# Kernel tuning notes

Measured on AMD Instinct MI355X. Metric: run time of the kernel, lower is better.

The kernel has to match this reference:

```python
import jax, jax.numpy as jnp
import numpy as np

N_NODES = 50000
N_EDGES = 640000  # directed; edges (2i, 2i+1) are mutual reverses
NODE_DIM = 128
EDGE_DIM = 16
UNITS = 128
EDGE_STEPS = 4
NODE_STEPS = 4


def setup_inputs() -> dict:
    key = jax.random.key(0)
    ks = jax.random.split(key, 8)
    n_pairs = N_EDGES // 2
    a = jax.random.randint(ks[0], (n_pairs,), 0, N_NODES, dtype=jnp.int32)
    b = jax.random.randint(ks[1], (n_pairs,), 0, N_NODES, dtype=jnp.int32)
    # interleave so edge 2i = a->b and edge 2i+1 = b->a (reverse pair)
    edge_src = jnp.stack([a, b], axis=1).reshape(-1)
    edge_dst = jnp.stack([b, a], axis=1).reshape(-1)
    rev_edge = (jnp.arange(N_EDGES, dtype=jnp.int32) ^ 1)
    node_feature = jax.random.normal(ks[2], (N_NODES, NODE_DIM), jnp.float32)
    edge_feature = jax.random.normal(ks[3], (N_EDGES, EDGE_DIM), jnp.float32)
    d_in = NODE_DIM + EDGE_DIM
    W_init = jax.random.normal(ks[4], (d_in, UNITS), jnp.float32) / np.sqrt(d_in)
    b_init = jnp.zeros((UNITS,), jnp.float32)
    W_upd = jax.random.normal(ks[5], (UNITS, UNITS), jnp.float32) / np.sqrt(UNITS)
    b_upd = jnp.zeros((UNITS,), jnp.float32)
    d_node_out = UNITS + NODE_DIM
    W_node = jax.random.normal(ks[6], (d_node_out, d_node_out), jnp.float32) / np.sqrt(d_node_out)
    b_node = jnp.zeros((d_node_out,), jnp.float32)
    epsilon = jnp.zeros((), jnp.float32)
    return dict(node_feature=node_feature, edge_feature=edge_feature,
                edge_src=edge_src, edge_dst=edge_dst, rev_edge=rev_edge,
                W_init=W_init, b_init=b_init, W_upd=W_upd, b_upd=b_upd,
                W_node=W_node, b_node=b_node, epsilon=epsilon)


def reference(node_feature, edge_feature, edge_src, edge_dst, rev_edge,
              W_init, b_init, W_upd, b_upd, W_node, b_node, epsilon):
    N = node_feature.shape[0]
    # initial edge projection: concat(src node feat, edge feat) -> units, relu
    h = jax.nn.relu(
        jnp.concatenate([node_feature[edge_src], edge_feature], axis=-1) @ W_init + b_init
    )  # [E, units]
    # directed edge message passing (D-MPNN style)
    for _ in range(EDGE_STEPS):
        agg = jax.ops.segment_sum(h, edge_dst, num_segments=N)        # [N, units]
        message = agg[edge_src] - h[rev_edge]                          # exclude reverse edge
        h = jax.nn.relu(message @ W_upd + b_upd + h)
    # aggregate edges to nodes, concat with original node features
    msg = jax.ops.segment_sum(h, edge_dst, num_segments=N)             # [N, units]
    x = jnp.concatenate([node_feature, msg], axis=-1)                  # [N, units+node_dim]
    x0 = (x * (1.0 + epsilon)) @ W_node + b_node                       # GIN-style initial
    # node message passing: sum-aggregate neighbors + residual initial
    for _ in range(NODE_STEPS):
        x = jax.ops.segment_sum(x[edge_src], edge_dst, num_segments=N) + x0
    return x
```

## Files before the change

### kernel.cpp

```cpp
#include <hip/hip_runtime.h>
#include <stdint.h>

#define N_NODES 50000
#define N_EDGES 640000
#define NODE_DIM 128
#define EDGE_DIM 16
#define UNITS 128
#define DOUT 256
#define SCAN_NB ((N_NODES + 255) / 256)

typedef __attribute__((ext_vector_type(4))) float v4f;
typedef __attribute__((ext_vector_type(8))) short v8s;
typedef __attribute__((ext_vector_type(4))) short v4s;
typedef __attribute__((ext_vector_type(2))) unsigned v2u;
typedef __attribute__((ext_vector_type(4))) unsigned v4u;

static __device__ __forceinline__ short f2bf(float f) {
    return (short)((__float_as_uint(f) + 0x8000u) >> 16);
}
static __device__ __forceinline__ float bf2f(short s) {
    return __uint_as_float(((unsigned)(unsigned short)s) << 16);
}
static __device__ __forceinline__ unsigned pack_bf2(float a, float b) {
    unsigned ua = __float_as_uint(a) + 0x8000u;
    unsigned ub = __float_as_uint(b) + 0x8000u;
    return __builtin_amdgcn_perm(ub, ua, 0x07060302);
}

__global__ void k_zero(int* __restrict__ p, int n) {
    int i = blockIdx.x * 256 + threadIdx.x;
    if (i < n) p[i] = 0;
}

__global__ void k_hist(const int* __restrict__ dst, int* __restrict__ counts) {
    int e = blockIdx.x * 256 + threadIdx.x;
    if (e < N_EDGES) atomicAdd(&counts[dst[e]], 1);
}

__global__ __launch_bounds__(256) void k_scan_part(const int* __restrict__ counts,
                                                   int* __restrict__ part) {
    __shared__ int red[256];
    int t = threadIdx.x;
    int i = blockIdx.x * 256 + t;
    red[t] = (i < N_NODES) ? counts[i] : 0;
    __syncthreads();
#pragma unroll
    for (int s = 128; s > 0; s >>= 1) {
        if (t < s) red[t] += red[t + s];
        __syncthreads();
    }
    if (t == 0) part[blockIdx.x] = red[0];
}

__global__ __launch_bounds__(256) void k_scan_base(const int* __restrict__ part,
                                                   int* __restrict__ base) {
    __shared__ int buf[2][256];
    int t = threadIdx.x;
    int v = (t < SCAN_NB) ? part[t] : 0;
    buf[0][t] = v;
    __syncthreads();
    int cur = 0;
#pragma unroll
    for (int s = 1; s < 256; s <<= 1) {
        int nv = buf[cur][t];
        if (t >= s) nv += buf[cur][t - s];
        buf[cur ^ 1][t] = nv;
        cur ^= 1;
        __syncthreads();
    }
    if (t < SCAN_NB) base[t] = buf[cur][t] - v;
}

__global__ __launch_bounds__(256) void k_scan_write(const int* __restrict__ counts,
                                                    const int* __restrict__ base,
                                                    int* __restrict__ rowptr,
                                                    int* __restrict__ cursor) {
    __shared__ int buf[2][256];
    int t = threadIdx.x;
    int i = blockIdx.x * 256 + t;
    int v = (i < N_NODES) ? counts[i] : 0;
    buf[0][t] = v;
    __syncthreads();
    int cur = 0;
#pragma unroll
    for (int s = 1; s < 256; s <<= 1) {
        int nv = buf[cur][t];
        if (t >= s) nv += buf[cur][t - s];
        buf[cur ^ 1][t] = nv;
        cur ^= 1;
        __syncthreads();
    }
    if (i < N_NODES) {
        int excl = buf[cur][t] - v + base[blockIdx.x];
        rowptr[i] = excl;
        cursor[i] = excl;
    }
    if (i == 0) rowptr[N_NODES] = N_EDGES;
}

__global__ void k_fill(const int* __restrict__ src, const int* __restrict__ dst,
                       int* __restrict__ cursor, int* __restrict__ csr_eid,
                       int* __restrict__ csr_src) {
    int e = blockIdx.x * 256 + threadIdx.x;
    if (e < N_EDGES) {
        int d = dst[e];
        int pos = atomicAdd(&cursor[d], 1);
        csr_eid[pos] = e;
        csr_src[pos] = src[e];
    }
}

__global__ void k_prep(const float* __restrict__ Wi, const float* __restrict__ Wu,
                       const float* __restrict__ Wn, short* __restrict__ WtI1,
                       short* __restrict__ WtI2, short* __restrict__ WtU,
                       short* __restrict__ WtN) {
    int i = blockIdx.x * 256 + threadIdx.x;
    if (i < 128 * 128) {
        int n = i >> 7, k = i & 127;
        WtI1[i] = f2bf(Wi[k * UNITS + n]);
        return;
    }
    int j = i - 128 * 128;
    if (j < 128 * 32) {
        int n = j >> 5, k = j & 31;
        WtI2[j] = (k < EDGE_DIM) ? f2bf(Wi[(NODE_DIM + k) * UNITS + n]) : (short)0;
        return;
    }
    int l = j - 128 * 32;
    if (l < 128 * 128) {
        int n = l >> 7, k = l & 127;
        WtU[l] = f2bf(Wu[k * UNITS + n]);
        return;
    }
    int m = l - 128 * 128;
    if (m < 256 * 256) {
        int n = m >> 8, k = m & 255;
        WtN[m] = f2bf(Wn[k * DOUT + n]);
    }
}

__global__ __launch_bounds__(256) void k_nfw(
    const float* __restrict__ nf, const short* __restrict__ WtI1,
    short* __restrict__ nfw) {
    __shared__ __align__(16) short nT[32][UNITS + 8];
    int t = threadIdx.x;
    int i0 = blockIdx.x * 32;
#pragma unroll
    for (int i = 0; i < 4; ++i) {
        int idx = i * 256 + t;
        int row = idx >> 5, c4 = idx & 31;
        int ri = i0 + row; if (ri >= N_NODES) ri = N_NODES - 1;
        v4f v = *(const v4f*)&nf[(size_t)ri * NODE_DIM + c4 * 4];
        unsigned* dst = (unsigned*)&nT[row][c4 * 4];
        dst[0] = pack_bf2(v[0], v[1]);
        dst[1] = pack_bf2(v[2], v[3]);
    }
    __syncthreads();
    int w = t >> 6, lane = t & 63, quad = lane >> 4, l16 = lane & 15;
    v4f acc[2][2];
#pragma unroll
    for (int m = 0; m < 2; ++m)
#pragma unroll
        for (int n = 0; n < 2; ++n) { acc[m][n][0] = 0; acc[m][n][1] = 0; acc[m][n][2] = 0; acc[m][n][3] = 0; }
#pragma unroll
    for (int kc = 0; kc < 4; ++kc) {
        int ko = kc * 32 + quad * 8;
        v8s a0 = *(const v8s*)&nT[l16][ko];
        v8s a1 = *(const v8s*)&nT[16 + l16][ko];
        v8s b0 = *(const v8s*)&WtI1[(size_t)(w * 32 + l16) * UNITS + ko];
        v8s b1 = *(const v8s*)&WtI1[(size_t)(w * 32 + 16 + l16) * UNITS + ko];
        acc[0][0] = __builtin_amdgcn_mfma_f32_16x16x32_bf16(a0, b0, acc[0][0], 0, 0, 0);
        acc[1][0] = __builtin_amdgcn_mfma_f32_16x16x32_bf16(a1, b0, acc[1][0], 0, 0, 0);
        acc[0][1] = __builtin_amdgcn_mfma_f32_16x16x32_bf16(a0, b1, acc[0][1], 0, 0, 0);
        acc[1][1] = __builtin_amdgcn_mfma_f32_16x16x32_bf16(a1, b1, acc[1][1], 0, 0, 0);
    }
#pragma unroll
    for (int m = 0; m < 2; ++m)
#pragma unroll
        for (int n = 0; n < 2; ++n)
#pragma unroll
            for (int r = 0; r < 4; ++r) {
                int row = m * 16 + quad * 4 + r;
                int col = w * 32 + n * 16 + l16;
                if (i0 + row < N_NODES)
                    nfw[(size_t)(i0 + row) * UNITS + col] = f2bf(acc[m][n][r]);
            }
}

__global__ __launch_bounds__(256) void k_edge_init2(
    const float* __restrict__ ef, const int* __restrict__ esrc,
    const short* __restrict__ nfw, const short* __restrict__ WtI2,
    const float* __restrict__ bi, short* __restrict__ h) {
    __shared__ __align__(16) short efT[32][40];
    __shared__ __align__(16) short nfwT[32][UNITS + 8];
    __shared__ int srcT[32];
    int t = threadIdx.x;
    int e0 = blockIdx.x * 32;
    if (t < 32) srcT[t] = esrc[e0 + t];
    if (t < 128) {
        int row = t >> 2, c4 = t & 3;
        v4f v = *(const v4f*)&ef[(size_t)(e0 + row) * EDGE_DIM + c4 * 4];
        unsigned* dst = (unsigned*)&efT[row][c4 * 4];
        dst[0] = pack_bf2(v[0], v[1]);
        dst[1] = pack_bf2(v[2], v[3]);
        unsigned* z = (unsigned*)&efT[row][16 + c4 * 4];
        z[0] = 0; z[1] = 0;
    }
    __syncthreads();
#pragma unroll
    for (int i = 0; i < 2; ++i) {
        int idx = i * 256 + t;
        int row = idx >> 4, c = idx & 15;
        v8s v = *(const v8s*)&nfw[(size_t)srcT[row] * UNITS + c * 8];
        *((v8s*)&nfwT[row][c * 8]) = v;
    }
    __syncthreads();
    int w = t >> 6, lane = t & 63, quad = lane >> 4, l16 = lane & 15;
    v4f acc[2][2];
#pragma unroll
    for (int m = 0; m < 2; ++m)
#pragma unroll
        for (int n = 0; n < 2; ++n) { acc[m][n][0] = 0; acc[m][n][1] = 0; acc[m][n][2] = 0; acc[m][n][3] = 0; }
    {
        int ko = quad * 8;
        v8s a0 = *(const v8s*)&efT[l16][ko];
        v8s a1 = *(const v8s*)&efT[16 + l16][ko];
        v8s b0 = *(const v8s*)&WtI2[(size_t)(w * 32 + l16) * 32 + ko];
        v8s b1 = *(const v8s*)&WtI2[(size_t)(w * 32 + 16 + l16) * 32 + ko];
        acc[0][0] = __builtin_amdgcn_mfma_f32_16x16x32_bf16(a0, b0, acc[0][0], 0, 0, 0);
        acc[1][0] = __builtin_amdgcn_mfma_f32_16x16x32_bf16(a1, b0, acc[1][0], 0, 0, 0);
        acc[0][1] = __builtin_amdgcn_mfma_f32_16x16x32_bf16(a0, b1, acc[0][1], 0, 0, 0);
        acc[1][1] = __builtin_amdgcn_mfma_f32_16x16x32_bf16(a1, b1, acc[1][1], 0, 0, 0);
    }
#pragma unroll
    for (int m = 0; m < 2; ++m)
#pragma unroll
        for (int n = 0; n < 2; ++n)
#pragma unroll
            for (int r = 0; r < 4; ++r) {
                int row = m * 16 + quad * 4 + r;
                int col = w * 32 + n * 16 + l16;
                float v = acc[m][n][r] + bf2f(nfwT[row][col]) + bi[col];
                h[(size_t)(e0 + row) * UNITS + col] = f2bf(fmaxf(v, 0.f));
            }
}

__global__ __launch_bounds__(256) void k_agg_bf(
    const short* __restrict__ h, const int* __restrict__ rowptr,
    const int* __restrict__ csr_eid, short* __restrict__ aggb) {
    int w = threadIdx.x >> 6, lane = threadIdx.x & 63;
    int node = blockIdx.x * 4 + w;
    int g = lane >> 4, l = lane & 15;
    int beg = rowptr[node], end = rowptr[node + 1];
    float a[8];
#pragma unroll
    for (int k = 0; k < 8; ++k) a[k] = 0.f;
    for (int j = beg + g; j < end; j += 4) {
        int eid = csr_eid[j];
        v8s u = *(const v8s*)&h[(size_t)eid * UNITS + l * 8];
#pragma unroll
        for (int k = 0; k < 8; ++k) a[k] += bf2f(u[k]);
    }
#pragma unroll
    for (int k = 0; k < 8; ++k) {
        a[k] += __shfl_xor(a[k], 16);
        a[k] += __shfl_xor(a[k], 32);
    }
    if (g == 0) {
        v4u o;
        o[0] = pack_bf2(a[0], a[1]); o[1] = pack_bf2(a[2], a[3]);
        o[2] = pack_bf2(a[4], a[5]); o[3] = pack_bf2(a[6], a[7]);
        *((v4u*)&aggb[(size_t)node * UNITS + l * 8]) = o;
    }
}

__global__ __launch_bounds__(256) void k_agg(
    const short* __restrict__ h, const int* __restrict__ rowptr,
    const int* __restrict__ csr_eid, float* __restrict__ agg) {
    int w = threadIdx.x >> 6, lane = threadIdx.x & 63;
    int node = blockIdx.x * 4 + w;
    int g = lane >> 4, l = lane & 15;
    int beg = rowptr[node], end = rowptr[node + 1];
    float a[8];
#pragma unroll
    for (int k = 0; k < 8; ++k) a[k] = 0.f;
    for (int j = beg + g; j < end; j += 4) {
        int eid = csr_eid[j];
        v8s u = *(const v8s*)&h[(size_t)eid * UNITS + l * 8];
#pragma unroll
        for (int k = 0; k < 8; ++k) a[k] += bf2f(u[k]);
    }
#pragma unroll
    for (int k = 0; k < 8; ++k) {
        a[k] += __shfl_xor(a[k], 16);
        a[k] += __shfl_xor(a[k], 32);
    }
    if (g == 0) {
        v4f o0, o1;
        o0[0] = a[0]; o0[1] = a[1]; o0[2] = a[2]; o0[3] = a[3];
        o1[0] = a[4]; o1[1] = a[5]; o1[2] = a[6]; o1[3] = a[7];
        *((v4f*)&agg[(size_t)node * UNITS + l * 8]) = o0;
        *((v4f*)&agg[(size_t)node * UNITS + l * 8 + 4]) = o1;
    }
}

__global__ __launch_bounds__(256, 4) void k_edge_step(
    const short* __restrict__ aggb, const int* __restrict__ esrc,
    const short* __restrict__ WtU, const float* __restrict__ bu,
    short* __restrict__ h) {
    __shared__ __align__(16) short hT[64][UNITS + 8];
    __shared__ __align__(16) short msgT[64][UNITS + 8];
    int t = threadIdx.x;
    int e0 = blockIdx.x * 64;
    int srcv[4];
#pragma unroll
    for (int i = 0; i < 4; ++i) srcv[i] = esrc[e0 + ((i * 256 + t) >> 4)];
    v8s hreg[4], areg[4];
#pragma unroll
    for (int i = 0; i < 4; ++i) {
        int idx = i * 256 + t;
        int row = idx >> 4, c = idx & 15;
        hreg[i] = *(const v8s*)&h[(size_t)(e0 + row) * UNITS + c * 8];
        areg[i] = *(const v8s*)&aggb[(size_t)srcv[i] * UNITS + c * 8];
    }
#pragma unroll
    for (int i = 0; i < 4; ++i) {
        int idx = i * 256 + t;
        int row = idx >> 4, c = idx & 15;
        *((v8s*)&hT[row][c * 8]) = hreg[i];
    }
    __syncthreads();
#pragma unroll
    for (int i = 0; i < 4; ++i) {
        int idx = i * 256 + t;
        int row = idx >> 4, c = idx & 15;
        v8s hr = *(const v8s*)&hT[row ^ 1][c * 8];
        unsigned* mrow = (unsigned*)&msgT[row][c * 8];
#pragma unroll
        for (int k = 0; k < 4; ++k) {
            float d0 = bf2f(areg[i][2 * k]) - bf2f(hr[2 * k]);
            float d1 = bf2f(areg[i][2 * k + 1]) - bf2f(hr[2 * k + 1]);
            mrow[k] = pack_bf2(d0, d1);
        }
    }
    __syncthreads();
    int w = t >> 6, lane = t & 63, quad = lane >> 4, l16 = lane & 15;
    v4f acc[4][2];
#pragma unroll
    for (int m = 0; m < 4; ++m)
#pragma unroll
        for (int n = 0; n < 2; ++n) { acc[m][n][0] = 0; acc[m][n][1] = 0; acc[m][n][2] = 0; acc[m][n][3] = 0; }
#pragma unroll
    for (int kc = 0; kc < 4; ++kc) {
        int ko = kc * 32 + quad * 8;
        v8s b0 = *(const v8s*)&WtU[(size_t)(w * 32 + l16) * UNITS + ko];
        v8s b1 = *(const v8s*)&WtU[(size_t)(w * 32 + 16 + l16) * UNITS + ko];
#pragma unroll
        for (int m = 0; m < 4; ++m) {
            v8s a = *(const v8s*)&msgT[m * 16 + l16][ko];
            acc[m][0] = __builtin_amdgcn_mfma_f32_16x16x32_bf16(a, b0, acc[m][0], 0, 0, 0);
            acc[m][1] = __builtin_amdgcn_mfma_f32_16x16x32_bf16(a, b1, acc[m][1], 0, 0, 0);
        }
    }
#pragma unroll
    for (int m = 0; m < 4; ++m)
#pragma unroll
        for (int n = 0; n < 2; ++n)
#pragma unroll
            for (int r = 0; r < 4; ++r) {
                int row = m * 16 + quad * 4 + r;
                int col = w * 32 + n * 16 + l16;
                float v = acc[m][n][r] + bu[col] + bf2f(hT[row][col]);
                hT[row][col] = f2bf(fmaxf(v, 0.f));
            }
    __syncthreads();
#pragma unroll
    for (int i = 0; i < 4; ++i) {
        int idx = i * 256 + t;
        int row = idx >> 4, c = idx & 15;
        *((v8s*)&h[(size_t)(e0 + row) * UNITS + c * 8]) = *(const v8s*)&hT[row][c * 8];
    }
}

__global__ __launch_bounds__(256) void k_node_init(
    const float* __restrict__ nf, const float* __restrict__ msg,
    const short* __restrict__ WtN, const float* __restrict__ bn,
    const float* __restrict__ epsv, float* __restrict__ x0,
    short* __restrict__ xcatb) {
    __shared__ __align__(16) short xin[32][DOUT + 8];
    int t = threadIdx.x;
    int i0 = blockIdx.x * 32;
#pragma unroll
    for (int i = 0; i < 8; ++i) {
        int idx = i * 256 + t;
        int row = idx >> 6, c4 = idx & 63;
        int ri = i0 + row; if (ri >= N_NODES) ri = N_NODES - 1;
        int col = c4 * 4;
        v4f v;
        if (col < NODE_DIM) v = *(const v4f*)&nf[(size_t)ri * NODE_DIM + col];
        else v = *(const v4f*)&msg[(size_t)ri * UNITS + (col - NODE_DIM)];
        unsigned* dst = (unsigned*)&xin[row][col];
        dst[0] = pack_bf2(v[0], v[1]);
        dst[1] = pack_bf2(v[2], v[3]);
    }
    __syncthreads();
#pragma unroll
    for (int i = 0; i < 4; ++i) {
        int idx = i * 256 + t;
        int row = idx >> 5, c = idx & 31;
        int ri = i0 + row;
        if (ri < N_NODES) {
            v8s v = *(const v8s*)&xin[row][c * 8];
            *((v8s*)&xcatb[(size_t)ri * DOUT + c * 8]) = v;
        }
    }
    int w = t >> 6, lane = t & 63, quad = lane >> 4, l16 = lane & 15;
    v4f acc[2][4];
#pragma unroll
    for (int m = 0; m < 2; ++m)
#pragma unroll
        for (int n = 0; n < 4; ++n) { acc[m][n][0] = 0; acc[m][n][1] = 0; acc[m][n][2] = 0; acc[m][n][3] = 0; }
#pragma unroll
    for (int kc = 0; kc < 8; ++kc) {
        int ko = kc * 32 + quad * 8;
        v8s a0 = *(const v8s*)&xin[l16][ko];
        v8s a1 = *(const v8s*)&xin[16 + l16][ko];
#pragma unroll
        for (int n = 0; n < 4; ++n) {
            v8s b = *(const v8s*)&WtN[(size_t)(w * 64 + n * 16 + l16) * DOUT + ko];
            acc[0][n] = __builtin_amdgcn_mfma_f32_16x16x32_bf16(a0, b, acc[0][n], 0, 0, 0);
            acc[1][n] = __builtin_amdgcn_mfma_f32_16x16x32_bf16(a1, b, acc[1][n], 0, 0, 0);
        }
    }
    float scale = 1.f + epsv[0];
#pragma unroll
    for (int m = 0; m < 2; ++m)
#pragma unroll
        for (int n = 0; n < 4; ++n)
#pragma unroll
            for (int r = 0; r < 4; ++r) {
                int row = m * 16 + quad * 4 + r;
                int col = w * 64 + n * 16 + l16;
                if (i0 + row < N_NODES)
                    x0[(size_t)(i0 + row) * DOUT + col] = acc[m][n][r] * scale + bn[col];
            }
}

__global__ __launch_bounds__(256) void k_node_step_b(
    const short* __restrict__ xb, const float* __restrict__ x0,
    const int* __restrict__ rowptr, const int* __restrict__ csr_src,
    short* __restrict__ outb, float* __restrict__ outf, int writef) {
    int w = threadIdx.x >> 6, lane = threadIdx.x & 63;
    int node = blockIdx.x * 4 + w;
    int beg = rowptr[node], end = rowptr[node + 1];
    v4f xv = *(const v4f*)&x0[(size_t)node * DOUT + lane * 4];
    float a0 = xv[0], a1 = xv[1], a2 = xv[2], a3 = xv[3];
    float b0 = 0, b1 = 0, b2 = 0, b3 = 0;
    int j = beg;
    for (; j + 2 <= end; j += 2) {
        int s0 = csr_src[j], s1 = csr_src[j + 1];
        v4s u = *(const v4s*)&xb[(size_t)s0 * DOUT + lane * 4];
        v4s v = *(const v4s*)&xb[(size_t)s1 * DOUT + lane * 4];
        a0 += bf2f(u[0]); a1 += bf2f(u[1]); a2 += bf2f(u[2]); a3 += bf2f(u[3]);
        b0 += bf2f(v[0]); b1 += bf2f(v[1]); b2 += bf2f(v[2]); b3 += bf2f(v[3]);
    }
    if (j < end) {
        v4s u = *(const v4s*)&xb[(size_t)csr_src[j] * DOUT + lane * 4];
        a0 += bf2f(u[0]); a1 += bf2f(u[1]); a2 += bf2f(u[2]); a3 += bf2f(u[3]);
    }
    a0 += b0; a1 += b1; a2 += b2; a3 += b3;
    if (writef) {
        v4f o; o[0] = a0; o[1] = a1; o[2] = a2; o[3] = a3;
        *((v4f*)&outf[(size_t)node * DOUT + lane * 4]) = o;
    } else {
        v2u o; o[0] = pack_bf2(a0, a1); o[1] = pack_bf2(a2, a3);
        *((v2u*)&outb[(size_t)node * DOUT + lane * 4]) = o;
    }
}

extern "C" void kernel_launch(void* const* d_in, const int* in_sizes, int n_in,
                              void* d_out, int out_size, void* d_ws, size_t ws_size,
                              hipStream_t stream) {
    const float* nf  = (const float*)d_in[0];
    const float* ef  = (const float*)d_in[1];
    const int* esrc  = (const int*)d_in[2];
    const int* edst  = (const int*)d_in[3];
    const float* Wi  = (const float*)d_in[5];
    const float* bi  = (const float*)d_in[6];
    const float* Wu  = (const float*)d_in[7];
    const float* bu  = (const float*)d_in[8];
    const float* Wn  = (const float*)d_in[9];
    const float* bn  = (const float*)d_in[10];
    const float* eps = (const float*)d_in[11];

    char* ws = (char*)d_ws;
    size_t off = 0;
    auto alloc = [&](size_t bytes) -> char* {
        char* p = ws + off;
        off += (bytes + 255) & ~(size_t)255;
        return p;
    };
    short* h     = (short*)alloc((size_t)N_EDGES * UNITS * 2);
    float* x0    = (float*)h;
    short* xcatb = (short*)((char*)h + (size_t)N_NODES * DOUT * 4);
    short* xbA   = (short*)((char*)xcatb + (size_t)N_NODES * DOUT * 2);
    short* xbB   = (short*)((char*)xbA + (size_t)N_NODES * DOUT * 2);
    char*  R     = alloc((size_t)N_NODES * UNITS * 4);
    short* nfw   = (short*)R;
    short* aggb  = (short*)(R + (size_t)N_NODES * UNITS * 2);
    float* agg   = (float*)R;
    int* counts  = (int*)alloc((size_t)N_NODES * 4);
    int* rowptr  = (int*)alloc((size_t)(N_NODES + 1) * 4);
    int* cursor  = (int*)alloc((size_t)N_NODES * 4);
    int* part    = (int*)alloc((size_t)SCAN_NB * 4);
    int* base    = (int*)alloc((size_t)SCAN_NB * 4);
    int* csr_eid = (int*)alloc((size_t)N_EDGES * 4);
    int* csr_src = (int*)alloc((size_t)N_EDGES * 4);
    short* WtI1  = (short*)alloc((size_t)128 * 128 * 2);
    short* WtI2  = (short*)alloc((size_t)128 * 32 * 2);
    short* WtU   = (short*)alloc((size_t)128 * 128 * 2);
    short* WtN   = (short*)alloc((size_t)256 * 256 * 2);
    float* xout  = (float*)d_out;

    if (ws_size < off) return;

    k_zero<<<(N_NODES + 255) / 256, 256, 0, stream>>>(counts, N_NODES);
    k_hist<<<(N_EDGES + 255) / 256, 256, 0, stream>>>(edst, counts);
    k_scan_part<<<SCAN_NB, 256, 0, stream>>>(counts, part);
    k_scan_base<<<1, 256, 0, stream>>>(part, base);
    k_scan_write<<<SCAN_NB, 256, 0, stream>>>(counts, base, rowptr, cursor);
    k_fill<<<(N_EDGES + 255) / 256, 256, 0, stream>>>(esrc, edst, cursor, csr_eid, csr_src);
    k_prep<<<(128 * 128 + 128 * 32 + 128 * 128 + 256 * 256 + 255) / 256, 256, 0, stream>>>(
        Wi, Wu, Wn, WtI1, WtI2, WtU, WtN);

    k_nfw<<<(N_NODES + 31) / 32, 256, 0, stream>>>(nf, WtI1, nfw);
    k_edge_init2<<<N_EDGES / 32, 256, 0, stream>>>(ef, esrc, nfw, WtI2, bi, h);
    for (int s = 0; s < 4; ++s) {
        k_agg_bf<<<N_NODES / 4, 256, 0, stream>>>(h, rowptr, csr_eid, aggb);
        k_edge_step<<<N_EDGES / 64, 256, 0, stream>>>(aggb, esrc, WtU, bu, h);
    }
    k_agg<<<N_NODES / 4, 256, 0, stream>>>(h, rowptr, csr_eid, agg);
    k_node_init<<<(N_NODES + 31) / 32, 256, 0, stream>>>(nf, agg, WtN, bn, eps, x0, xcatb);
    k_node_step_b<<<N_NODES / 4, 256, 0, stream>>>(xcatb, x0, rowptr, csr_src, xbA, nullptr, 0);
    k_node_step_b<<<N_NODES / 4, 256, 0, stream>>>(xbA, x0, rowptr, csr_src, xbB, nullptr, 0);
    k_node_step_b<<<N_NODES / 4, 256, 0, stream>>>(xbB, x0, rowptr, csr_src, xbA, nullptr, 0);
    k_node_step_b<<<N_NODES / 4, 256, 0, stream>>>(xbA, x0, rowptr, csr_src, nullptr, xout, 1);
}
```

Before: 1.025 ms.

## Stage GEMM outputs through LDS for coalesced stores and preload CSR indices via shuffles

k_nfw and k_edge_init2 now write their accumulator tiles to shared memory and store rows to global memory as 16-byte vectors instead of scattered 2-byte stores. k_edge_init2 also doubles its tile to 64 edges and issues its gathered neighbor loads before the edge-feature conversion. The aggregation and node-step kernels load up to 64 CSR indices in one coalesced read and broadcast them with shuffles, keeping more gathers in flight per iteration. This adds LDS traffic, extra barriers and a separate fallback path for nodes with degree above 64.

```diff
diff --git a/kernel.cpp b/kernel.cpp
--- a/kernel.cpp
+++ b/kernel.cpp
@@ -174,6 +174,7 @@
         acc[0][1] = __builtin_amdgcn_mfma_f32_16x16x32_bf16(a0, b1, acc[0][1], 0, 0, 0);
         acc[1][1] = __builtin_amdgcn_mfma_f32_16x16x32_bf16(a1, b1, acc[1][1], 0, 0, 0);
     }
+    __syncthreads();
 #pragma unroll
     for (int m = 0; m < 2; ++m)
 #pragma unroll
@@ -182,22 +183,36 @@
             for (int r = 0; r < 4; ++r) {
                 int row = m * 16 + quad * 4 + r;
                 int col = w * 32 + n * 16 + l16;
-                if (i0 + row < N_NODES)
-                    nfw[(size_t)(i0 + row) * UNITS + col] = f2bf(acc[m][n][r]);
+                nT[row][col] = f2bf(acc[m][n][r]);
             }
+    __syncthreads();
+#pragma unroll
+    for (int i = 0; i < 2; ++i) {
+        int idx = i * 256 + t;
+        int row = idx >> 4, c = idx & 15;
+        if (i0 + row < N_NODES)
+            *((v8s*)&nfw[(size_t)(i0 + row) * UNITS + c * 8]) = *(const v8s*)&nT[row][c * 8];
+    }
 }
 
 __global__ __launch_bounds__(256) void k_edge_init2(
     const float* __restrict__ ef, const int* __restrict__ esrc,
     const short* __restrict__ nfw, const short* __restrict__ WtI2,
     const float* __restrict__ bi, short* __restrict__ h) {
-    __shared__ __align__(16) short efT[32][40];
-    __shared__ __align__(16) short nfwT[32][UNITS + 8];
-    __shared__ int srcT[32];
+    __shared__ __align__(16) short efT[64][40];
+    __shared__ __align__(16) short nfwT[64][UNITS + 8];
     int t = threadIdx.x;
-    int e0 = blockIdx.x * 32;
-    if (t < 32) srcT[t] = esrc[e0 + t];
-    if (t < 128) {
+    int e0 = blockIdx.x * 64;
+    int r0 = t >> 4, c = t & 15;
+    int s0 = esrc[e0 + r0];
+    int s1 = esrc[e0 + 16 + r0];
+    int s2 = esrc[e0 + 32 + r0];
+    int s3 = esrc[e0 + 48 + r0];
+    v8s n0 = *(const v8s*)&nfw[(size_t)s0 * UNITS + c * 8];
+    v8s n1 = *(const v8s*)&nfw[(size_t)s1 * UNITS + c * 8];
+    v8s n2 = *(const v8s*)&nfw[(size_t)s2 * UNITS + c * 8];
+    v8s n3 = *(const v8s*)&nfw[(size_t)s3 * UNITS + c * 8];
+    {
         int row = t >> 2, c4 = t & 3;
         v4f v = *(const v4f*)&ef[(size_t)(e0 + row) * EDGE_DIM + c4 * 4];
         unsigned* dst = (unsigned*)&efT[row][c4 * 4];
@@ -206,34 +221,30 @@
         unsigned* z = (unsigned*)&efT[row][16 + c4 * 4];
         z[0] = 0; z[1] = 0;
     }
-    __syncthreads();
-#pragma unroll
-    for (int i = 0; i < 2; ++i) {
-        int idx = i * 256 + t;
-        int row = idx >> 4, c = idx & 15;
-        v8s v = *(const v8s*)&nfw[(size_t)srcT[row] * UNITS + c * 8];
-        *((v8s*)&nfwT[row][c * 8]) = v;
-    }
+    *((v8s*)&nfwT[r0][c * 8]) = n0;
+    *((v8s*)&nfwT[16 + r0][c * 8]) = n1;
+    *((v8s*)&nfwT[32 + r0][c * 8]) = n2;
+    *((v8s*)&nfwT[48 + r0][c * 8]) = n3;
     __syncthreads();
     int w = t >> 6, lane = t & 63, quad = lane >> 4, l16 = lane & 15;
-    v4f acc[2][2];
-#pragma unroll
-    for (int m = 0; m < 2; ++m)
+    v4f acc[4][2];
+#pragma unroll
+    for (int m = 0; m < 4; ++m)
 #pragma unroll
         for (int n = 0; n < 2; ++n) { acc[m][n][0] = 0; acc[m][n][1] = 0; acc[m][n][2] = 0; acc[m][n][3] = 0; }
     {
         int ko = quad * 8;
-        v8s a0 = *(const v8s*)&efT[l16][ko];
-        v8s a1 = *(const v8s*)&efT[16 + l16][ko];
         v8s b0 = *(const v8s*)&WtI2[(size_t)(w * 32 + l16) * 32 + ko];
         v8s b1 = *(const v8s*)&WtI2[(size_t)(w * 32 + 16 + l16) * 32 + ko];
-        acc[0][0] = __builtin_amdgcn_mfma_f32_16x16x32_bf16(a0, b0, acc[0][0], 0, 0, 0);
-        acc[1][0] = __builtin_amdgcn_mfma_f32_16x16x32_bf16(a1, b0, acc[1][0], 0, 0, 0);
-        acc[0][1] = __builtin_amdgcn_mfma_f32_16x16x32_bf16(a0, b1, acc[0][1], 0, 0, 0);
-        acc[1][1] = __builtin_amdgcn_mfma_f32_16x16x32_bf16(a1, b1, acc[1][1], 0, 0, 0);
-    }
-#pragma unroll
-    for (int m = 0; m < 2; ++m)
+#pragma unroll
+        for (int m = 0; m < 4; ++m) {
+            v8s a = *(const v8s*)&efT[m * 16 + l16][ko];
+            acc[m][0] = __builtin_amdgcn_mfma_f32_16x16x32_bf16(a, b0, acc[m][0], 0, 0, 0);
+            acc[m][1] = __builtin_amdgcn_mfma_f32_16x16x32_bf16(a, b1, acc[m][1], 0, 0, 0);
+        }
+    }
+#pragma unroll
+    for (int m = 0; m < 4; ++m)
 #pragma unroll
         for (int n = 0; n < 2; ++n)
 #pragma unroll
@@ -241,8 +252,15 @@
                 int row = m * 16 + quad * 4 + r;
                 int col = w * 32 + n * 16 + l16;
                 float v = acc[m][n][r] + bf2f(nfwT[row][col]) + bi[col];
-                h[(size_t)(e0 + row) * UNITS + col] = f2bf(fmaxf(v, 0.f));
+                nfwT[row][col] = f2bf(fmaxf(v, 0.f));
             }
+    __syncthreads();
+#pragma unroll
+    for (int i = 0; i < 4; ++i) {
+        int idx = i * 256 + t;
+        int row = idx >> 4, cc = idx & 15;
+        *((v8s*)&h[(size_t)(e0 + row) * UNITS + cc * 8]) = *(const v8s*)&nfwT[row][cc * 8];
+    }
 }
 
 __global__ __launch_bounds__(256) void k_agg_bf(
@@ -252,12 +270,30 @@
     int node = blockIdx.x * 4 + w;
     int g = lane >> 4, l = lane & 15;
     int beg = rowptr[node], end = rowptr[node + 1];
+    int deg = end - beg;
+    int ev = (lane < deg) ? csr_eid[beg + lane] : 0;
+    int dcap = deg < 64 ? deg : 64;
     float a[8];
 #pragma unroll
     for (int k = 0; k < 8; ++k) a[k] = 0.f;
-    for (int j = beg + g; j < end; j += 4) {
-        int eid = csr_eid[j];
-        v8s u = *(const v8s*)&h[(size_t)eid * UNITS + l * 8];
+    for (int base = 0; base < dcap; base += 8) {
+        int j0 = base + g, j1 = j0 + 4;
+        int ea = __shfl(ev, j0);
+        int eb = __shfl(ev, j1);
+        if (j1 < dcap) {
+            v8s u = *(const v8s*)&h[(size_t)ea * UNITS + l * 8];
+            v8s v = *(const v8s*)&h[(size_t)eb * UNITS + l * 8];
+#pragma unroll
+            for (int k = 0; k < 8; ++k) a[k] += bf2f(u[k]) + bf2f(v[k]);
+        } else if (j0 < dcap) {
+            v8s u = *(const v8s*)&h[(size_t)ea * UNITS + l * 8];
+#pragma unroll
+            for (int k = 0; k < 8; ++k) a[k] += bf2f(u[k]);
+        }
+    }
+    for (int jj = 64 + g; jj < deg; jj += 4) {
+        int ea = csr_eid[beg + jj];
+        v8s u = *(const v8s*)&h[(size_t)ea * UNITS + l * 8];
 #pragma unroll
         for (int k = 0; k < 8; ++k) a[k] += bf2f(u[k]);
     }
@@ -281,12 +317,30 @@
     int node = blockIdx.x * 4 + w;
     int g = lane >> 4, l = lane & 15;
     int beg = rowptr[node], end = rowptr[node + 1];
+    int deg = end - beg;
+    int ev = (lane < deg) ? csr_eid[beg + lane] : 0;
+    int dcap = deg < 64 ? deg : 64;
     float a[8];
 #pragma unroll
     for (int k = 0; k < 8; ++k) a[k] = 0.f;
-    for (int j = beg + g; j < end; j += 4) {
-        int eid = csr_eid[j];
-        v8s u = *(const v8s*)&h[(size_t)eid * UNITS + l * 8];
+    for (int base = 0; base < dcap; base += 8) {
+        int j0 = base + g, j1 = j0 + 4;
+        int ea = __shfl(ev, j0);
+        int eb = __shfl(ev, j1);
+        if (j1 < dcap) {
+            v8s u = *(const v8s*)&h[(size_t)ea * UNITS + l * 8];
+            v8s v = *(const v8s*)&h[(size_t)eb * UNITS + l * 8];
+#pragma unroll
+            for (int k = 0; k < 8; ++k) a[k] += bf2f(u[k]) + bf2f(v[k]);
+        } else if (j0 < dcap) {
+            v8s u = *(const v8s*)&h[(size_t)ea * UNITS + l * 8];
+#pragma unroll
+            for (int k = 0; k < 8; ++k) a[k] += bf2f(u[k]);
+        }
+    }
+    for (int jj = 64 + g; jj < deg; jj += 4) {
+        int ea = csr_eid[beg + jj];
+        v8s u = *(const v8s*)&h[(size_t)ea * UNITS + l * 8];
 #pragma unroll
         for (int k = 0; k < 8; ++k) a[k] += bf2f(u[k]);
     }
@@ -453,20 +507,34 @@
     int w = threadIdx.x >> 6, lane = threadIdx.x & 63;
     int node = blockIdx.x * 4 + w;
     int beg = rowptr[node], end = rowptr[node + 1];
+    int deg = end - beg;
+    int sv = (lane < deg) ? csr_src[beg + lane] : 0;
+    int dcap = deg < 64 ? deg : 64;
     v4f xv = *(const v4f*)&x0[(size_t)node * DOUT + lane * 4];
     float a0 = xv[0], a1 = xv[1], a2 = xv[2], a3 = xv[3];
     float b0 = 0, b1 = 0, b2 = 0, b3 = 0;
-    int j = beg;
-    for (; j + 2 <= end; j += 2) {
-        int s0 = csr_src[j], s1 = csr_src[j + 1];
-        v4s u = *(const v4s*)&xb[(size_t)s0 * DOUT + lane * 4];
-        v4s v = *(const v4s*)&xb[(size_t)s1 * DOUT + lane * 4];
-        a0 += bf2f(u[0]); a1 += bf2f(u[1]); a2 += bf2f(u[2]); a3 += bf2f(u[3]);
-        b0 += bf2f(v[0]); b1 += bf2f(v[1]); b2 += bf2f(v[2]); b3 += bf2f(v[3]);
-    }
-    if (j < end) {
-        v4s u = *(const v4s*)&xb[(size_t)csr_src[j] * DOUT + lane * 4];
-        a0 += bf2f(u[0]); a1 += bf2f(u[1]); a2 += bf2f(u[2]); a3 += bf2f(u[3]);
+    int j = 0;
+    for (; j + 4 <= dcap; j += 4) {
+        int s0 = __shfl(sv, j), s1 = __shfl(sv, j + 1);
+        int s2 = __shfl(sv, j + 2), s3 = __shfl(sv, j + 3);
+        v4s u0 = *(const v4s*)&xb[(size_t)s0 * DOUT + lane * 4];
+        v4s u1 = *(const v4s*)&xb[(size_t)s1 * DOUT + lane * 4];
+        v4s u2 = *(const v4s*)&xb[(size_t)s2 * DOUT + lane * 4];
+        v4s u3 = *(const v4s*)&xb[(size_t)s3 * DOUT + lane * 4];
+        a0 += bf2f(u0[0]) + bf2f(u1[0]); b0 += bf2f(u2[0]) + bf2f(u3[0]);
+        a1 += bf2f(u0[1]) + bf2f(u1[1]); b1 += bf2f(u2[1]) + bf2f(u3[1]);
+        a2 += bf2f(u0[2]) + bf2f(u1[2]); b2 += bf2f(u2[2]) + bf2f(u3[2]);
+        a3 += bf2f(u0[3]) + bf2f(u1[3]); b3 += bf2f(u2[3]) + bf2f(u3[3]);
+    }
+    for (; j < dcap; ++j) {
+        int s0 = __shfl(sv, j);
+        v4s u0 = *(const v4s*)&xb[(size_t)s0 * DOUT + lane * 4];
+        a0 += bf2f(u0[0]); a1 += bf2f(u0[1]); a2 += bf2f(u0[2]); a3 += bf2f(u0[3]);
+    }
+    for (int jj = 64; jj < deg; ++jj) {
+        int s0 = csr_src[beg + jj];
+        v4s u0 = *(const v4s*)&xb[(size_t)s0 * DOUT + lane * 4];
+        a0 += bf2f(u0[0]); a1 += bf2f(u0[1]); a2 += bf2f(u0[2]); a3 += bf2f(u0[3]);
     }
     a0 += b0; a1 += b1; a2 += b2; a3 += b3;
     if (writef) {
@@ -534,7 +602,7 @@
         Wi, Wu, Wn, WtI1, WtI2, WtU, WtN);
 
     k_nfw<<<(N_NODES + 31) / 32, 256, 0, stream>>>(nf, WtI1, nfw);
-    k_edge_init2<<<N_EDGES / 32, 256, 0, stream>>>(ef, esrc, nfw, WtI2, bi, h);
+    k_edge_init2<<<N_EDGES / 64, 256, 0, stream>>>(ef, esrc, nfw, WtI2, bi, h);
     for (int s = 0; s < 4; ++s) {
         k_agg_bf<<<N_NODES / 4, 256, 0, stream>>>(h, rowptr, csr_eid, aggb);
         k_edge_step<<<N_EDGES / 64, 256, 0, stream>>>(aggb, esrc, WtU, bu, h);
```

New measurement: 968.9 us. -5.4%, faster.
